# Kernel tuning notes

Measured on AMD Instinct MI355X. Metric: run time of the kernel, lower is better.

Reference implementation:

```python
import jax, jax.numpy as jnp
import numpy as np

B, S, H, D = 2, 4096, 16, 128  # batch, seq, heads, head_dim
HID = H * D                    # 2048 hidden size
C = 128                        # chunk size for the chunked recurrent scan
EPS = 1e-6


def setup_inputs() -> dict:
    key = jax.random.key(0)
    ks = jax.random.split(key, 9)
    sc = 0.02  # initializer_range
    w = lambda k: jax.random.normal(k, (HID, HID), jnp.float32) * sc
    return {
        "x": jax.random.normal(ks[0], (B, S, HID), jnp.float32),
        "Wq": w(ks[1]), "bq": jnp.zeros((HID,), jnp.float32),
        "Wk": w(ks[2]), "bk": jnp.zeros((HID,), jnp.float32),
        "Wv": w(ks[3]), "bv": jnp.zeros((HID,), jnp.float32),
        "Wo": w(ks[4]), "bo": jnp.zeros((HID,), jnp.float32),
    }


def reference(x, Wq, bq, Wk, bk, Wv, bv, Wo, bo):
    Bx, Sx, hid = x.shape
    NC = Sx // C  # number of chunks

    q = (x @ Wq + bq).reshape(Bx, Sx, H, D)
    k = (x @ Wk + bk).reshape(Bx, Sx, H, D)
    v = (x @ Wv + bv).reshape(Bx, Sx, H, D)

    # positive feature map for linear attention
    qf = jax.nn.elu(q) + 1.0
    kf = jax.nn.elu(k) + 1.0

    # chunk: [B, NC, C, H, D]
    qf = qf.reshape(Bx, NC, C, H, D)
    kf = kf.reshape(Bx, NC, C, H, D)
    vc = v.reshape(Bx, NC, C, H, D)

    # inter-chunk recurrent state: exclusive cumulative sums of per-chunk KV outer
    kv = jnp.einsum('bnchd,bnche->bnhde', kf, vc)      # per-chunk KV state
    kv_ex = jnp.cumsum(kv, axis=1) - kv                # exclusive prefix state
    ksum = kf.sum(axis=2)                              # [B,NC,H,D]
    ksum_ex = jnp.cumsum(ksum, axis=1) - ksum          # exclusive normalizer state

    inter = jnp.einsum('bnchd,bnhde->bnche', qf, kv_ex)
    z_inter = jnp.einsum('bnchd,bnhd->bnch', qf, ksum_ex)

    # intra-chunk causal attention (masked matmul)
    A = jnp.einsum('bnchd,bnkhd->bnhck', qf, kf)       # [B,NC,H,C,C]
    causal = jnp.tril(jnp.ones((C, C), dtype=bool))
    A = jnp.where(causal[None, None, None], A, 0.0)
    intra = jnp.einsum('bnhck,bnkhe->bnche', A, vc)
    z_intra = jnp.swapaxes(A.sum(-1), 2, 3)            # [B,NC,C,H]

    out = (inter + intra) / (z_inter + z_intra + EPS)[..., None]
    out = out.reshape(Bx, Sx, hid)
    return out @ Wo + bo
```

## Files before the change

### kernel.cpp

```cpp
#include <hip/hip_runtime.h>

typedef unsigned short u16;
typedef unsigned int u32;
typedef unsigned long long u64;
typedef __attribute__((ext_vector_type(8))) short short8;
typedef __attribute__((ext_vector_type(4))) float f32x4;
typedef __attribute__((ext_vector_type(4))) int int4v;

constexpr int Bsz = 2, Ssz = 4096, Hn = 16, Dh = 128, HID = 2048;
constexpr int Cch = 128, NCh = 32;
constexpr float EPSf = 1e-6f;

#define MFMA16 __builtin_amdgcn_mfma_f32_16x16x32_bf16
#define VMCNT4 asm volatile("s_waitcnt vmcnt(4)" ::: "memory")
#define VMCNT0 asm volatile("s_waitcnt vmcnt(0)" ::: "memory")

__device__ __forceinline__ float b2f(u16 u) {
  unsigned int i = ((unsigned int)u) << 16;
  return __builtin_bit_cast(float, i);
}
__device__ __forceinline__ u16 f2b(float f) {
  unsigned int i = __builtin_bit_cast(unsigned int, f);
  i += 0x7fffu + ((i >> 16) & 1u);
  return (u16)(i >> 16);
}

__device__ __forceinline__ void gload_lds16(const u16* g, u16* l) {
  __builtin_amdgcn_global_load_lds(
      (const __attribute__((address_space(1))) u32*)g,
      (__attribute__((address_space(3))) u32*)l, 16, 0, 0);
}

__global__ __launch_bounds__(256) void cvt_bf16(const float* __restrict__ x,
                                                u16* __restrict__ xb)
{
  const size_t n8 = (size_t)Bsz * Ssz * HID / 8;
  for (size_t i = (size_t)blockIdx.x * 256 + threadIdx.x; i < n8;
       i += (size_t)gridDim.x * 256) {
    const f32x4 a = *(const f32x4*)&x[i * 8];
    const f32x4 b = *(const f32x4*)&x[i * 8 + 4];
    u16 tmp[8];
#pragma unroll
    for (int u = 0; u < 4; ++u) { tmp[u] = f2b(a[u]); tmp[u + 4] = f2b(b[u]); }
    *(int4v*)&xb[i * 8] = *(const int4v*)tmp;
  }
}

__global__ __launch_bounds__(256) void transpose4(
    const float* __restrict__ A0, const float* __restrict__ A1,
    const float* __restrict__ A2, const float* __restrict__ A3,
    u16* __restrict__ T0, u16* __restrict__ T1,
    u16* __restrict__ T2, u16* __restrict__ T3)
{
  constexpr int N = HID, LDT = 72;
  const int z = blockIdx.z;
  const float* __restrict__ A = (z == 0) ? A0 : (z == 1) ? A1 : (z == 2) ? A2 : A3;
  u16* __restrict__ T = (z == 0) ? T0 : (z == 1) ? T1 : (z == 2) ? T2 : T3;
  __shared__ u16 lds[64 * LDT];
  const int t = threadIdx.x;
  const int i = t >> 3, j = (t & 7) * 8;
  const int r0 = blockIdx.y * 64, c0 = blockIdx.x * 64;
#pragma unroll
  for (int half = 0; half < 2; ++half) {
    const int r = i + half * 32;
    const f32x4 a = *(const f32x4*)&A[(size_t)(r0 + r) * N + c0 + j];
    const f32x4 b = *(const f32x4*)&A[(size_t)(r0 + r) * N + c0 + j + 4];
    u16 tmp[8];
#pragma unroll
    for (int u = 0; u < 4; ++u) { tmp[u] = f2b(a[u]); tmp[u + 4] = f2b(b[u]); }
    *(int4v*)&lds[r * LDT + j] = *(const int4v*)tmp;
  }
  __syncthreads();
#pragma unroll
  for (int half = 0; half < 2; ++half) {
    const int c = i + half * 32;
    u16 tmp[8];
#pragma unroll
    for (int u = 0; u < 8; ++u) tmp[u] = lds[(j + u) * LDT + c];
    *(int4v*)&T[(size_t)(c0 + c) * N + r0 + j] = *(const int4v*)tmp;
  }
}

template <int OUTF32>
__global__ __launch_bounds__(512) void gemm2b(
    const u16* __restrict__ A,
    const u16* __restrict__ W0T, const u16* __restrict__ W1T, const u16* __restrict__ W2T,
    const float* __restrict__ bb0, const float* __restrict__ bb1, const float* __restrict__ bb2,
    void* __restrict__ o0, void* __restrict__ o1, void* __restrict__ o2,
    int elu_mask)
{
  constexpr int K = HID, N = HID;
  constexpr int NT = K / 64;
  extern __shared__ u16 lds[];

  const int z = blockIdx.z;
  const u16* __restrict__ WT    = (z == 0) ? W0T : (z == 1) ? W1T : W2T;
  const float* __restrict__ bias = (z == 0) ? bb0 : (z == 1) ? bb1 : bb2;
  void* __restrict__ outv = (z == 0) ? o0 : (z == 1) ? o1 : o2;
  const bool elu = (elu_mask >> z) & 1;

  const int lid = blockIdx.x + 8 * blockIdx.y;
  const int wlid = (lid & 7) * 32 + (lid >> 3);
  const int n0 = (wlid >> 5) * 256;
  const int m0 = (wlid & 31) * 256;

  const int t = threadIdx.x, lane = t & 63, w = t >> 6;
  const int wm = w >> 2, wn = w & 3;
  const int l15 = lane & 15, lg = lane >> 4;
  const int sl2 = (l15 >> 1) & 3;

  const int strow = lane >> 2;
  const int stslot = (lane & 3) ^ ((lane >> 3) & 3);
  const u16* gA = A  + (size_t)(m0 + w * 16 + strow) * K + stslot * 8;
  const u16* gB = WT + (size_t)(n0 + w * 16 + strow) * K + stslot * 8;

  const int aRow = (wm * 128 + l15) * 32 + ((lg ^ sl2) << 3);
  const int bRow = 16384 + (wn * 64 + l15) * 32 + ((lg ^ sl2) << 3);
  u16* const lw = &lds[w * 512];

  f32x4 acc[8][4] = {};
  short8 aF[8], bF[4];

#define STAGE(SB, KKC) do {                                                   \
    gload_lds16(gA + (KKC) * 32,                 lw + (SB)*32768 + (KKC)*8192);          \
    gload_lds16(gA + (KKC) * 32 + (size_t)128*K, lw + (SB)*32768 + (KKC)*8192 + 4096);   \
    gload_lds16(gB + (KKC) * 32,                 lw + (SB)*32768 + 16384 + (KKC)*8192);  \
    gload_lds16(gB + (KKC) * 32 + (size_t)128*K, lw + (SB)*32768 + 16384 + (KKC)*8192 + 4096); \
  } while (0)

#define HALF(BUF, KKC, PF) do {                                               \
    _Pragma("unroll")                                                         \
    for (int i = 0; i < 8; ++i)                                               \
      aF[i] = *(const short8*)&lds[(BUF)*32768 + (KKC)*8192 + aRow + i*512];  \
    _Pragma("unroll")                                                         \
    for (int j = 0; j < 4; ++j)                                               \
      bF[j] = *(const short8*)&lds[(BUF)*32768 + (KKC)*8192 + bRow + j*512];  \
    if (PF) STAGE((BUF)^1, KKC);                                              \
    __builtin_amdgcn_s_setprio(1);                                            \
    _Pragma("unroll")                                                         \
    for (int i = 0; i < 8; ++i) {                                             \
      acc[i][0] = MFMA16(aF[i], bF[0], acc[i][0], 0, 0, 0);                   \
      acc[i][1] = MFMA16(aF[i], bF[1], acc[i][1], 0, 0, 0);                   \
      acc[i][2] = MFMA16(aF[i], bF[2], acc[i][2], 0, 0, 0);                   \
      acc[i][3] = MFMA16(aF[i], bF[3], acc[i][3], 0, 0, 0);                   \
    }                                                                         \
    __builtin_amdgcn_s_setprio(0);                                            \
  } while (0)

  STAGE(0, 0);
  STAGE(0, 1);
  gA += 64; gB += 64;
  VMCNT4;
  __builtin_amdgcn_s_barrier();

  for (int W = 0; W < NT; W += 2) {
    const bool p0 = (W + 1) < NT, p1 = (W + 2) < NT;
    HALF(0, 0, p0);
    if (p0) { VMCNT4; } else { VMCNT0; }
    __builtin_amdgcn_s_barrier();
    HALF(0, 1, p0);
    if (p0) { gA += 64; gB += 64; VMCNT4; __builtin_amdgcn_s_barrier(); }
    if (p0) {
      HALF(1, 0, p1);
      if (p1) { VMCNT4; } else { VMCNT0; }
      __builtin_amdgcn_s_barrier();
      HALF(1, 1, p1);
      if (p1) { gA += 64; gB += 64; VMCNT4; __builtin_amdgcn_s_barrier(); }
    }
  }

#pragma unroll
  for (int j = 0; j < 4; ++j) {
    const int col = n0 + wn * 64 + j * 16 + l15;
    const float bv = bias[col];
#pragma unroll
    for (int i = 0; i < 8; ++i) {
      const int row0 = m0 + wm * 128 + i * 16 + lg * 4;
#pragma unroll
      for (int r = 0; r < 4; ++r) {
        float v = acc[i][j][r] + bv;
        if (elu) v = (v > 0.0f) ? (v + 1.0f) : __expf(v);
        if (OUTF32) ((float*)outv)[(size_t)(row0 + r) * N + col] = v;
        else        ((u16*)outv)[(size_t)(row0 + r) * N + col] = f2b(v);
      }
    }
  }
#undef STAGE
#undef HALF
}

__global__ __launch_bounds__(256) void pass1_kv(
    const u16* __restrict__ KF, const u16* __restrict__ V,
    u16* __restrict__ KVT, float* __restrict__ KSUM)
{
  constexpr int LD = 136;
  __shared__ u16 lk[128 * LD];
  __shared__ u16 lv[128 * LD];
  const int bnh = blockIdx.x;
  const int h = bnh % Hn, n = (bnh / Hn) % NCh, b = bnh / (Hn * NCh);
  const size_t rowbase = (size_t)(b * Ssz + n * Cch) * HID + h * Dh;
  const int t = threadIdx.x, lane = t & 63, w = t >> 6;
  const int wr = (w >> 1) * 64, wc = (w & 1) * 64;
  const int l15 = lane & 15, lg = lane >> 4;
  const int sr = t >> 4, sc = (t & 15) * 8;

#pragma unroll
  for (int rep = 0; rep < 8; ++rep) {
    const int r = rep * 16 + sr;
    *(int4v*)&lk[r * LD + sc] = *(const int4v*)&KF[rowbase + (size_t)r * HID + sc];
    *(int4v*)&lv[r * LD + sc] = *(const int4v*)&V[rowbase + (size_t)r * HID + sc];
  }
  __syncthreads();

  if (t < 128) {
    float s = 0.0f;
    for (int c = 0; c < 128; ++c) s += b2f(lk[c * LD + t]);
    KSUM[(size_t)bnh * Dh + t] = s;
  }

  f32x4 acc[4][4] = {};
#pragma unroll
  for (int kk = 0; kk < 4; ++kk) {
    const int cb = kk * 32 + lg * 8;
    short8 aF[4], bF[4];
#pragma unroll
    for (int i = 0; i < 4; ++i) {
      const int e = wr + i * 16 + l15;
      short8 a;
#pragma unroll
      for (int u = 0; u < 8; ++u) a[u] = (short)lv[(cb + u) * LD + e];
      aF[i] = a;
    }
#pragma unroll
    for (int j = 0; j < 4; ++j) {
      const int d = wc + j * 16 + l15;
      short8 bb;
#pragma unroll
      for (int u = 0; u < 8; ++u) bb[u] = (short)lk[(cb + u) * LD + d];
      bF[j] = bb;
    }
#pragma unroll
    for (int i = 0; i < 4; ++i)
#pragma unroll
      for (int j = 0; j < 4; ++j)
        acc[i][j] = MFMA16(aF[i], bF[j], acc[i][j], 0, 0, 0);
  }

  u16* __restrict__ outp = KVT + (size_t)bnh * (Dh * Dh);
#pragma unroll
  for (int i = 0; i < 4; ++i) {
    const int e0 = wr + i * 16 + lg * 4;
#pragma unroll
    for (int j = 0; j < 4; ++j) {
      const int d = wc + j * 16 + l15;
#pragma unroll
      for (int r = 0; r < 4; ++r)
        outp[(size_t)(e0 + r) * Dh + d] = f2b(acc[i][j][r]);
    }
  }
}

__global__ __launch_bounds__(256) void cumsum_kv(u16* __restrict__ KVT) {
  const int tid = blockIdx.x * 256 + threadIdx.x;
  const int ed = tid & (Dh * Dh - 1);
  const int bh = tid >> 14;
  const int h = bh % Hn, b = bh / Hn;
  const size_t base = ((size_t)(b * NCh * Hn) + h) * (Dh * Dh) + ed;
  const size_t stride = (size_t)Hn * Dh * Dh;
  float s = 0.0f;
  for (int n = 0; n < NCh; ++n) {
    const size_t idx = base + (size_t)n * stride;
    const float v = b2f(KVT[idx]);
    KVT[idx] = f2b(s);
    s += v;
  }
}

__global__ __launch_bounds__(256) void cumsum_ks(float* __restrict__ KS) {
  const int tid = blockIdx.x * 256 + threadIdx.x;
  const int d = tid & (Dh - 1);
  const int bh = tid >> 7;
  const int h = bh % Hn, b = bh / Hn;
  const size_t base = ((size_t)(b * NCh * Hn) + h) * Dh + d;
  const size_t stride = (size_t)Hn * Dh;
  float s = 0.0f;
  for (int n = 0; n < NCh; ++n) {
    const size_t idx = base + (size_t)n * stride;
    const float v = KS[idx];
    KS[idx] = s;
    s += v;
  }
}

__global__ __launch_bounds__(256) void pass2_attn(
    const u16* __restrict__ QF, const u16* __restrict__ KF, const u16* __restrict__ V,
    const u16* __restrict__ KVT, const float* __restrict__ KSE,
    u16* __restrict__ Y)
{
  constexpr int LD = 136;
  __shared__ u16 smem[4 * 128 * LD];
  __shared__ float zbuf[128];
  u16* sQ  = smem;
  u16* sK  = smem + 128 * LD;
  u16* sA  = smem + 2 * 128 * LD;
  u16* sKV = smem + 3 * 128 * LD;

  const int bnh = blockIdx.x;
  const int h = bnh % Hn, n = (bnh / Hn) % NCh, b = bnh / (Hn * NCh);
  const size_t rowbase = (size_t)(b * Ssz + n * Cch) * HID + h * Dh;
  const int t = threadIdx.x, lane = t & 63, w = t >> 6;
  const int wr = (w >> 1) * 64, wc = (w & 1) * 64;
  const int l15 = lane & 15, lg = lane >> 4;
  const int sr = t >> 4, sc = (t & 15) * 8;

  const u16* __restrict__ kvsrc = KVT + (size_t)bnh * (Dh * Dh);
#pragma unroll
  for (int rep = 0; rep < 8; ++rep) {
    const int r = rep * 16 + sr;
    *(int4v*)&sQ[r * LD + sc]  = *(const int4v*)&QF[rowbase + (size_t)r * HID + sc];
    *(int4v*)&sK[r * LD + sc]  = *(const int4v*)&KF[rowbase + (size_t)r * HID + sc];
    *(int4v*)&sKV[r * LD + sc] = *(const int4v*)&kvsrc[r * Dh + sc];
  }
  __syncthreads();

  f32x4 acc[4][4] = {};
#pragma unroll
  for (int kk = 0; kk < 4; ++kk) {
    const int krd = kk * 32 + lg * 8;
    short8 aF[4], bF[4];
#pragma unroll
    for (int i = 0; i < 4; ++i)
      aF[i] = *(const short8*)&sQ[(wr + i * 16 + l15) * LD + krd];
#pragma unroll
    for (int j = 0; j < 4; ++j)
      bF[j] = *(const short8*)&sK[(wc + j * 16 + l15) * LD + krd];
#pragma unroll
    for (int i = 0; i < 4; ++i)
#pragma unroll
      for (int j = 0; j < 4; ++j)
        acc[i][j] = MFMA16(aF[i], bF[j], acc[i][j], 0, 0, 0);
  }
#pragma unroll
  for (int i = 0; i < 4; ++i) {
    const int c0 = wr + i * 16 + lg * 4;
#pragma unroll
    for (int j = 0; j < 4; ++j) {
      const int ck = wc + j * 16 + l15;
#pragma unroll
      for (int r = 0; r < 4; ++r) {
        const int c = c0 + r;
        sA[c * LD + ck] = f2b((ck <= c) ? acc[i][j][r] : 0.0f);
      }
    }
  }
  __syncthreads();

  if (t < 128) {
    const float* kse = KSE + (size_t)bnh * Dh;
    float zz = EPSf;
    for (int d2 = 0; d2 < 128; ++d2) zz += b2f(sQ[t * LD + d2]) * kse[d2];
    for (int ck = 0; ck < 128; ++ck) zz += b2f(sA[t * LD + ck]);
    zbuf[t] = zz;
  }
#pragma unroll
  for (int rep = 0; rep < 8; ++rep) {
    const int r = rep * 16 + sr;
    *(int4v*)&sK[r * LD + sc] = *(const int4v*)&V[rowbase + (size_t)r * HID + sc];
  }
  __syncthreads();

  f32x4 o[4][4] = {};
#pragma unroll
  for (int kk = 0; kk < 4; ++kk) {
    const int krd = kk * 32 + lg * 8;
    short8 aF[4], bF[4];
#pragma unroll
    for (int i = 0; i < 4; ++i)
      aF[i] = *(const short8*)&sA[(wr + i * 16 + l15) * LD + krd];
#pragma unroll
    for (int j = 0; j < 4; ++j) {
      const int e = wc + j * 16 + l15;
      short8 bb;
#pragma unroll
      for (int u = 0; u < 8; ++u) bb[u] = (short)sK[(krd + u) * LD + e];
      bF[j] = bb;
    }
#pragma unroll
    for (int i = 0; i < 4; ++i)
#pragma unroll
      for (int j = 0; j < 4; ++j)
        o[i][j] = MFMA16(aF[i], bF[j], o[i][j], 0, 0, 0);
  }
#pragma unroll
  for (int kk = 0; kk < 4; ++kk) {
    const int krd = kk * 32 + lg * 8;
    short8 aF[4], bF[4];
#pragma unroll
    for (int i = 0; i < 4; ++i)
      aF[i] = *(const short8*)&sQ[(wr + i * 16 + l15) * LD + krd];
#pragma unroll
    for (int j = 0; j < 4; ++j)
      bF[j] = *(const short8*)&sKV[(wc + j * 16 + l15) * LD + krd];
#pragma unroll
    for (int i = 0; i < 4; ++i)
#pragma unroll
      for (int j = 0; j < 4; ++j)
        o[i][j] = MFMA16(aF[i], bF[j], o[i][j], 0, 0, 0);
  }

#pragma unroll
  for (int i = 0; i < 4; ++i) {
    const int c0 = wr + i * 16 + lg * 4;
#pragma unroll
    for (int j = 0; j < 4; ++j) {
      const int e = wc + j * 16 + l15;
#pragma unroll
      for (int r = 0; r < 4; ++r) {
        const int c = c0 + r;
        Y[rowbase + (size_t)c * HID + e] = f2b(o[i][j][r] / zbuf[c]);
      }
    }
  }
}

extern "C" void kernel_launch(void* const* d_in, const int* in_sizes, int n_in,
                              void* d_out, int out_size, void* d_ws, size_t ws_size,
                              hipStream_t stream)
{
  const float* x  = (const float*)d_in[0];
  const float* Wq = (const float*)d_in[1];
  const float* bq = (const float*)d_in[2];
  const float* Wk = (const float*)d_in[3];
  const float* bk = (const float*)d_in[4];
  const float* Wv = (const float*)d_in[5];
  const float* bv = (const float*)d_in[6];
  const float* Wo = (const float*)d_in[7];
  const float* bo = (const float*)d_in[8];
  float* out = (float*)d_out;

  char* p = (char*)d_ws;
  auto take = [&](size_t bytes) { char* q = p; p += (bytes + 255) & ~(size_t)255; return q; };
  u16* WqT = (u16*)take((size_t)HID * HID * 2);
  u16* WkT = (u16*)take((size_t)HID * HID * 2);
  u16* WvT = (u16*)take((size_t)HID * HID * 2);
  u16* WoT = (u16*)take((size_t)HID * HID * 2);
  u16* QF  = (u16*)take((size_t)Bsz * Ssz * HID * 2);
  u16* KFb = (u16*)take((size_t)Bsz * Ssz * HID * 2);
  u16* Vb  = (u16*)take((size_t)Bsz * Ssz * HID * 2);
  char* region = take((size_t)Bsz * Ssz * HID * 2);
  u16* xb  = (u16*)region;
  u16* KVT = (u16*)region;
  float* KS = (float*)take((size_t)Bsz * NCh * Hn * Dh * 4);
  u16* Yb = QF;

  (void)hipFuncSetAttribute((const void*)gemm2b<0>,
                            hipFuncAttributeMaxDynamicSharedMemorySize, 131072);
  (void)hipFuncSetAttribute((const void*)gemm2b<1>,
                            hipFuncAttributeMaxDynamicSharedMemorySize, 131072);

  dim3 blk(256, 1, 1);
  cvt_bf16<<<dim3(2048), blk, 0, stream>>>(x, xb);
  transpose4<<<dim3(HID / 64, HID / 64, 4), blk, 0, stream>>>(
      Wq, Wk, Wv, Wo, WqT, WkT, WvT, WoT);
  gemm2b<0><<<dim3(HID / 256, (Bsz * Ssz) / 256, 3), dim3(512), 131072, stream>>>(
      xb, WqT, WkT, WvT, bq, bk, bv, QF, KFb, Vb, 0x3);
  pass1_kv<<<dim3(Bsz * NCh * Hn), blk, 0, stream>>>(KFb, Vb, KVT, KS);
  cumsum_kv<<<dim3((Bsz * Hn * Dh * Dh) / 256), blk, 0, stream>>>(KVT);
  cumsum_ks<<<dim3((Bsz * Hn * Dh) / 256), blk, 0, stream>>>(KS);
  pass2_attn<<<dim3(Bsz * NCh * Hn), blk, 0, stream>>>(QF, KFb, Vb, KVT, KS, Yb);
  gemm2b<1><<<dim3(HID / 256, (Bsz * Ssz) / 256, 1), dim3(512), 131072, stream>>>(
      Yb, WoT, WoT, WoT, bo, bo, bo, out, out, out, 0);
}
```

Before: 418.5 us.

## Coarsen GEMM pipeline to one barrier per window, merge cumsums, split reductions

The GEMM main loop now does one wait-all and barrier per 64-wide K window, then prefetches the whole next window before computing on the current one. Before, it had finer half-window waits with vmcnt(4). The two cumsum kernels are merged into one launch to save a launch. The KSUM column sum in pass1 and the normalizer sums in pass2 are split across all 256 threads instead of 128. The coarser GEMM sync removes some barriers, but the loads for the next window now have only one window of compute to hide behind.

```diff
diff --git a/kernel.cpp b/kernel.cpp
--- a/kernel.cpp
+++ b/kernel.cpp
@@ -12,7 +12,6 @@
 constexpr float EPSf = 1e-6f;
 
 #define MFMA16 __builtin_amdgcn_mfma_f32_16x16x32_bf16
-#define VMCNT4 asm volatile("s_waitcnt vmcnt(4)" ::: "memory")
 #define VMCNT0 asm volatile("s_waitcnt vmcnt(0)" ::: "memory")
 
 __device__ __forceinline__ float b2f(u16 u) {
@@ -82,7 +81,7 @@
 }
 
 template <int OUTF32>
-__global__ __launch_bounds__(512) void gemm2b(
+__global__ __launch_bounds__(512) void gemm1b(
     const u16* __restrict__ A,
     const u16* __restrict__ W0T, const u16* __restrict__ W1T, const u16* __restrict__ W2T,
     const float* __restrict__ bb0, const float* __restrict__ bb1, const float* __restrict__ bb2,
@@ -128,14 +127,13 @@
     gload_lds16(gB + (KKC) * 32 + (size_t)128*K, lw + (SB)*32768 + 16384 + (KKC)*8192 + 4096); \
   } while (0)
 
-#define HALF(BUF, KKC, PF) do {                                               \
+#define HALFBODY(BUF, KKC) do {                                               \
     _Pragma("unroll")                                                         \
     for (int i = 0; i < 8; ++i)                                               \
       aF[i] = *(const short8*)&lds[(BUF)*32768 + (KKC)*8192 + aRow + i*512];  \
     _Pragma("unroll")                                                         \
     for (int j = 0; j < 4; ++j)                                               \
       bF[j] = *(const short8*)&lds[(BUF)*32768 + (KKC)*8192 + bRow + j*512];  \
-    if (PF) STAGE((BUF)^1, KKC);                                              \
     __builtin_amdgcn_s_setprio(1);                                            \
     _Pragma("unroll")                                                         \
     for (int i = 0; i < 8; ++i) {                                             \
@@ -147,26 +145,21 @@
     __builtin_amdgcn_s_setprio(0);                                            \
   } while (0)
 
+#define WINDOW(BUF, PF) do {                                                  \
+    VMCNT0;                                                                   \
+    __builtin_amdgcn_s_barrier();                                             \
+    if (PF) { STAGE((BUF)^1, 0); STAGE((BUF)^1, 1); gA += 64; gB += 64; }     \
+    HALFBODY(BUF, 0);                                                         \
+    HALFBODY(BUF, 1);                                                         \
+  } while (0)
+
   STAGE(0, 0);
   STAGE(0, 1);
   gA += 64; gB += 64;
-  VMCNT4;
-  __builtin_amdgcn_s_barrier();
 
   for (int W = 0; W < NT; W += 2) {
-    const bool p0 = (W + 1) < NT, p1 = (W + 2) < NT;
-    HALF(0, 0, p0);
-    if (p0) { VMCNT4; } else { VMCNT0; }
-    __builtin_amdgcn_s_barrier();
-    HALF(0, 1, p0);
-    if (p0) { gA += 64; gB += 64; VMCNT4; __builtin_amdgcn_s_barrier(); }
-    if (p0) {
-      HALF(1, 0, p1);
-      if (p1) { VMCNT4; } else { VMCNT0; }
-      __builtin_amdgcn_s_barrier();
-      HALF(1, 1, p1);
-      if (p1) { gA += 64; gB += 64; VMCNT4; __builtin_amdgcn_s_barrier(); }
-    }
+    WINDOW(0, (W + 1) < NT);
+    WINDOW(1, (W + 2) < NT);
   }
 
 #pragma unroll
@@ -186,7 +179,8 @@
     }
   }
 #undef STAGE
-#undef HALF
+#undef HALFBODY
+#undef WINDOW
 }
 
 __global__ __launch_bounds__(256) void pass1_kv(
@@ -196,6 +190,7 @@
   constexpr int LD = 136;
   __shared__ u16 lk[128 * LD];
   __shared__ u16 lv[128 * LD];
+  __shared__ float kp[256];
   const int bnh = blockIdx.x;
   const int h = bnh % Hn, n = (bnh / Hn) % NCh, b = bnh / (Hn * NCh);
   const size_t rowbase = (size_t)(b * Ssz + n * Cch) * HID + h * Dh;
@@ -212,11 +207,14 @@
   }
   __syncthreads();
 
-  if (t < 128) {
+  {
+    const int col = t & 127, hf = t >> 7;
     float s = 0.0f;
-    for (int c = 0; c < 128; ++c) s += b2f(lk[c * LD + t]);
-    KSUM[(size_t)bnh * Dh + t] = s;
-  }
+    for (int c = hf * 64; c < hf * 64 + 64; ++c) s += b2f(lk[c * LD + col]);
+    kp[t] = s;
+  }
+  __syncthreads();
+  if (t < 128) KSUM[(size_t)bnh * Dh + t] = kp[t] + kp[t + 128];
 
   f32x4 acc[4][4] = {};
 #pragma unroll
@@ -260,35 +258,38 @@
   }
 }
 
-__global__ __launch_bounds__(256) void cumsum_kv(u16* __restrict__ KVT) {
-  const int tid = blockIdx.x * 256 + threadIdx.x;
-  const int ed = tid & (Dh * Dh - 1);
-  const int bh = tid >> 14;
-  const int h = bh % Hn, b = bh / Hn;
-  const size_t base = ((size_t)(b * NCh * Hn) + h) * (Dh * Dh) + ed;
-  const size_t stride = (size_t)Hn * Dh * Dh;
-  float s = 0.0f;
-  for (int n = 0; n < NCh; ++n) {
-    const size_t idx = base + (size_t)n * stride;
-    const float v = b2f(KVT[idx]);
-    KVT[idx] = f2b(s);
-    s += v;
-  }
-}
-
-__global__ __launch_bounds__(256) void cumsum_ks(float* __restrict__ KS) {
-  const int tid = blockIdx.x * 256 + threadIdx.x;
-  const int d = tid & (Dh - 1);
-  const int bh = tid >> 7;
-  const int h = bh % Hn, b = bh / Hn;
-  const size_t base = ((size_t)(b * NCh * Hn) + h) * Dh + d;
-  const size_t stride = (size_t)Hn * Dh;
-  float s = 0.0f;
-  for (int n = 0; n < NCh; ++n) {
-    const size_t idx = base + (size_t)n * stride;
-    const float v = KS[idx];
-    KS[idx] = s;
-    s += v;
+__global__ __launch_bounds__(256) void cumsum_all(u16* __restrict__ KVT,
+                                                  float* __restrict__ KS)
+{
+  const int nkv = (Bsz * Hn * Dh * Dh) / 256;
+  if ((int)blockIdx.x < nkv) {
+    const int tid = blockIdx.x * 256 + threadIdx.x;
+    const int ed = tid & (Dh * Dh - 1);
+    const int bh = tid >> 14;
+    const int h = bh % Hn, b = bh / Hn;
+    const size_t base = ((size_t)(b * NCh * Hn) + h) * (Dh * Dh) + ed;
+    const size_t stride = (size_t)Hn * Dh * Dh;
+    float s = 0.0f;
+    for (int n = 0; n < NCh; ++n) {
+      const size_t idx = base + (size_t)n * stride;
+      const float v = b2f(KVT[idx]);
+      KVT[idx] = f2b(s);
+      s += v;
+    }
+  } else {
+    const int tid = (blockIdx.x - nkv) * 256 + threadIdx.x;
+    const int d = tid & (Dh - 1);
+    const int bh = tid >> 7;
+    const int h = bh % Hn, b = bh / Hn;
+    const size_t base = ((size_t)(b * NCh * Hn) + h) * Dh + d;
+    const size_t stride = (size_t)Hn * Dh;
+    float s = 0.0f;
+    for (int n = 0; n < NCh; ++n) {
+      const size_t idx = base + (size_t)n * stride;
+      const float v = KS[idx];
+      KS[idx] = s;
+      s += v;
+    }
   }
 }
 
@@ -299,7 +300,7 @@
 {
   constexpr int LD = 136;
   __shared__ u16 smem[4 * 128 * LD];
-  __shared__ float zbuf[128];
+  __shared__ float zpart[2][128];
   u16* sQ  = smem;
   u16* sK  = smem + 128 * LD;
   u16* sA  = smem + 2 * 128 * LD;
@@ -357,10 +358,14 @@
 
   if (t < 128) {
     const float* kse = KSE + (size_t)bnh * Dh;
-    float zz = EPSf;
+    float zz = 0.0f;
     for (int d2 = 0; d2 < 128; ++d2) zz += b2f(sQ[t * LD + d2]) * kse[d2];
-    for (int ck = 0; ck < 128; ++ck) zz += b2f(sA[t * LD + ck]);
-    zbuf[t] = zz;
+    zpart[0][t] = zz;
+  } else {
+    const int row = t - 128;
+    float zz = 0.0f;
+    for (int ck = 0; ck < 128; ++ck) zz += b2f(sA[row * LD + ck]);
+    zpart[1][row] = zz;
   }
 #pragma unroll
   for (int rep = 0; rep < 8; ++rep) {
@@ -417,7 +422,8 @@
 #pragma unroll
       for (int r = 0; r < 4; ++r) {
         const int c = c0 + r;
-        Y[rowbase + (size_t)c * HID + e] = f2b(o[i][j][r] / zbuf[c]);
+        const float zz = zpart[0][c] + zpart[1][c] + EPSf;
+        Y[rowbase + (size_t)c * HID + e] = f2b(o[i][j][r] / zz);
       }
     }
   }
@@ -453,21 +459,20 @@
   float* KS = (float*)take((size_t)Bsz * NCh * Hn * Dh * 4);
   u16* Yb = QF;
 
-  (void)hipFuncSetAttribute((const void*)gemm2b<0>,
+  (void)hipFuncSetAttribute((const void*)gemm1b<0>,
                             hipFuncAttributeMaxDynamicSharedMemorySize, 131072);
-  (void)hipFuncSetAttribute((const void*)gemm2b<1>,
+  (void)hipFuncSetAttribute((const void*)gemm1b<1>,
                             hipFuncAttributeMaxDynamicSharedMemorySize, 131072);
 
   dim3 blk(256, 1, 1);
   cvt_bf16<<<dim3(2048), blk, 0, stream>>>(x, xb);
   transpose4<<<dim3(HID / 64, HID / 64, 4), blk, 0, stream>>>(
       Wq, Wk, Wv, Wo, WqT, WkT, WvT, WoT);
-  gemm2b<0><<<dim3(HID / 256, (Bsz * Ssz) / 256, 3), dim3(512), 131072, stream>>>(
+  gemm1b<0><<<dim3(HID / 256, (Bsz * Ssz) / 256, 3), dim3(512), 131072, stream>>>(
       xb, WqT, WkT, WvT, bq, bk, bv, QF, KFb, Vb, 0x3);
   pass1_kv<<<dim3(Bsz * NCh * Hn), blk, 0, stream>>>(KFb, Vb, KVT, KS);
-  cumsum_kv<<<dim3((Bsz * Hn * Dh * Dh) / 256), blk, 0, stream>>>(KVT);
-  cumsum_ks<<<dim3((Bsz * Hn * Dh) / 256), blk, 0, stream>>>(KS);
+  cumsum_all<<<dim3((Bsz * Hn * Dh * Dh) / 256 + (Bsz * Hn * Dh) / 256), blk, 0, stream>>>(KVT, KS);
   pass2_attn<<<dim3(Bsz * NCh * Hn), blk, 0, stream>>>(QF, KFb, Vb, KVT, KS, Yb);
-  gemm2b<1><<<dim3(HID / 256, (Bsz * Ssz) / 256, 1), dim3(512), 131072, stream>>>(
+  gemm1b<1><<<dim3(HID / 256, (Bsz * Ssz) / 256, 1), dim3(512), 131072, stream>>>(
       Yb, WoT, WoT, WoT, bo, bo, bo, out, out, out, 0);
 }
```

New measurement: 421.0 us. Within noise of the previous version (+0.6%).
